# Kernel optimization log

Measured on AMD Instinct MI355X. Metric: run time of the kernel, lower is better.

Reference implementation:

```python
import jax, jax.numpy as jnp
import numpy as np

N_NODES = 50000
IN_CH = 128
OUT_CH = 64
HID = 2 * OUT_CH  # 128
N_EDGES = 800000


def _glorot(key, shape):
    fan_in, fan_out = shape[0], shape[-1]
    lim = jnp.sqrt(6.0 / (fan_in + fan_out))
    return jax.random.uniform(key, shape, jnp.float32, -lim, lim)


def setup_inputs() -> dict:
    key = jax.random.key(0)
    ks = jax.random.split(key, 10)
    x = jax.random.normal(ks[0], (N_NODES, IN_CH), jnp.float32)
    edge_index = jax.random.randint(ks[1], (2, N_EDGES), 0, N_NODES, jnp.int32)
    return {
        "x": x,
        "edge_index": edge_index,
        "W1": _glorot(ks[2], (IN_CH, HID)),
        "a_src1": _glorot(ks[3], (HID,)),
        "a_dst1": _glorot(ks[4], (HID,)),
        "b1": jnp.zeros((HID,), jnp.float32),
        "W2": _glorot(ks[5], (HID, OUT_CH)),
        "a_src2": _glorot(ks[6], (OUT_CH,)),
        "a_dst2": _glorot(ks[7], (OUT_CH,)),
        "b2": jnp.zeros((OUT_CH,), jnp.float32),
    }


def _gat_conv(x, src, dst, W, a_src, a_dst, b, n_nodes):
    # Linear transform: [N, F_out]
    h = x @ W
    # Per-node attention halves (heads=1): alpha_i = <h_i, a>
    al_s = h @ a_src  # [N]
    al_d = h @ a_dst  # [N]
    # Edge scores with LeakyReLU(0.2), PyG default negative slope
    e = jax.nn.leaky_relu(al_s[src] + al_d[dst], negative_slope=0.2)
    # Segment softmax over incoming edges of each dst node
    m = jax.ops.segment_max(e, dst, num_segments=n_nodes)
    m = jnp.where(jnp.isfinite(m), m, 0.0)
    ex = jnp.exp(e - m[dst])
    denom = jax.ops.segment_sum(ex, dst, num_segments=n_nodes)
    alpha = ex / (denom[dst] + 1e-16)  # [E]
    # Weighted scatter-add aggregation
    out = jax.ops.segment_sum(h[src] * alpha[:, None], dst, num_segments=n_nodes)
    return out + b


def reference(x, edge_index, W1, a_src1, a_dst1, b1, W2, a_src2, a_dst2, b2):
    n = x.shape[0]
    # add_self_loops=True (PyG GATConv default)
    loops = jnp.arange(n, dtype=edge_index.dtype)
    src = jnp.concatenate([edge_index[0], loops])
    dst = jnp.concatenate([edge_index[1], loops])
    h = _gat_conv(x.astype(jnp.float32), src, dst, W1, a_src1, a_dst1, b1, n)
    h = jax.nn.relu(h)
    return _gat_conv(h, src, dst, W2, a_src2, a_dst2, b2, n)
```

## Files before the change

kernel.cpp:

```cpp
#include <hip/hip_runtime.h>
#include <hip/hip_bf16.h>

#define N_NODES 50000
#define IN_CH 128
#define HID 128
#define OUT_CH 64
#define N_EDGES 800000
#define N_TOT_EDGES (N_EDGES + N_NODES)
#define ET_PAD (N_TOT_EDGES + 3 * N_NODES)
#define MPAD 50048
#define NBN ((N_NODES + 255) / 256)
#define NB_ET ((N_TOT_EDGES + 255) / 256)
#define NB_GEMM (MPAD / 64)
#define NSH 128
#define EPS (N_EDGES / NSH)
#define NDW (N_NODES / 4)

typedef float float4v __attribute__((ext_vector_type(4)));
typedef unsigned uint4v __attribute__((ext_vector_type(4)));
typedef __attribute__((ext_vector_type(8))) short bf16x8;
typedef __attribute__((ext_vector_type(4))) float f32x4;

__device__ __forceinline__ unsigned bf16_rne(float f) {
    unsigned u = __float_as_uint(f);
    return (u + 0x7fffu + ((u >> 16) & 1u)) >> 16;
}
__device__ __forceinline__ unsigned pack2(float a, float b) {
    return bf16_rne(a) | (bf16_rne(b) << 16);
}

__global__ __launch_bounds__(256) void k_pre(
        const float* __restrict__ W1, unsigned short* __restrict__ Wl1,
        const float* __restrict__ W2, unsigned short* __restrict__ Wl2) {
    const int b = blockIdx.x, t = threadIdx.x;
    const float* W; unsigned short* Wl; int N, bb;
    if (b < 8) { W = W1; Wl = Wl1; N = 128; bb = b; }
    else       { W = W2; Wl = Wl2; N = 64;  bb = b - 8; }
    const int tg = bb * 256 + t;
    if (tg >= 16 * N) return;
    const int kg = tg / N, col = tg & (N - 1);
    float v[8];
    #pragma unroll
    for (int j = 0; j < 8; ++j) v[j] = W[(size_t)(kg * 8 + j) * N + col];
    uint4 p;
    p.x = pack2(v[0], v[1]); p.y = pack2(v[2], v[3]);
    p.z = pack2(v[4], v[5]); p.w = pack2(v[6], v[7]);
    *(uint4*)&Wl[(size_t)tg * 8] = p;
}

template<int N, bool AF32, bool USELDS>
__device__ __forceinline__ void gemm_body(int gb, int t,
        const float* __restrict__ Xf, const unsigned short* __restrict__ Xb,
        const unsigned short* __restrict__ Wlg,
        const float* __restrict__ asrc, const float* __restrict__ adst,
        unsigned short* __restrict__ Hb, float* __restrict__ als,
        float* __restrict__ ald, int M, unsigned short* Wl) {
    constexpr int NF = N / 16;
    const unsigned short* Wsrc;
    if constexpr (USELDS) {
        for (int i = t; i < N * 16; i += 256)
            ((uint4*)Wl)[i] = ((const uint4*)Wlg)[i];
        __syncthreads();
        Wsrc = Wl;
    } else {
        Wsrc = Wlg;
    }

    const int lane = t & 63, w = t >> 6;
    const int rb = gb * 64 + w * 16;
    const int cl = lane & 15, g = lane >> 4;

    f32x4 acc[NF];
    #pragma unroll
    for (int n = 0; n < NF; ++n) acc[n] = (f32x4){0.f, 0.f, 0.f, 0.f};

    const float* Xrow = nullptr;
    const unsigned short* Abase = nullptr;
    if constexpr (AF32) {
        const int arow = (rb + cl < M) ? (rb + cl) : (M - 1);
        Xrow = Xf + (size_t)arow * 128;
    } else {
        Abase = Xb + (size_t)(rb >> 4) * 2048 + cl * 8;
    }

    #pragma unroll
    for (int s = 0; s < 4; ++s) {
        bf16x8 af;
        if constexpr (AF32) {
            const int k0 = (s * 4 + g) * 8;
            float4 a = *(const float4*)&Xrow[k0];
            float4 c = *(const float4*)&Xrow[k0 + 4];
            uint4v uu;
            uu[0] = pack2(a.x, a.y); uu[1] = pack2(a.z, a.w);
            uu[2] = pack2(c.x, c.y); uu[3] = pack2(c.z, c.w);
            af = __builtin_bit_cast(bf16x8, uu);
        } else {
            af = *(const bf16x8*)(Abase + (s * 4 + g) * 128);
        }
        #pragma unroll
        for (int n = 0; n < NF; ++n) {
            bf16x8 bf = *(const bf16x8*)(Wsrc + ((s * 4 + g) * N + n * 16 + cl) * 8);
            acc[n] = __builtin_amdgcn_mfma_f32_16x16x32_bf16(af, bf, acc[n], 0, 0, 0);
        }
    }

    float asv[NF], adv[NF];
    #pragma unroll
    for (int n = 0; n < NF; ++n) {
        asv[n] = asrc[n * 16 + cl];
        adv[n] = adst[n * 16 + cl];
    }

    #pragma unroll
    for (int r = 0; r < 4; ++r) {
        float ps = 0.f, pd = 0.f;
        #pragma unroll
        for (int n = 0; n < NF; ++n) {
            ps += acc[n][r] * asv[n];
            pd += acc[n][r] * adv[n];
        }
        #pragma unroll
        for (int mask = 1; mask < 16; mask <<= 1) {
            ps += __shfl_xor(ps, mask);
            pd += __shfl_xor(pd, mask);
        }
        const int row = rb + g * 4 + r;
        if (cl == 0 && row < M) { als[row] = ps; ald[row] = pd; }
    }

    #pragma unroll
    for (int r = 0; r < 4; ++r) {
        const int row = rb + g * 4 + r;
        if (row >= M) continue;
        #pragma unroll
        for (int n = 0; n < NF; ++n)
            Hb[(size_t)(n >> 1) * (size_t)M * 32 + (size_t)row * 32
               + (n & 1) * 16 + cl] = (unsigned short)bf16_rne(acc[n][r]);
    }
}

__global__ __launch_bounds__(256) void k_par1(
        const int* __restrict__ ei, unsigned* __restrict__ cnt_s,
        unsigned char* __restrict__ rank8,
        const float* __restrict__ X, const unsigned short* __restrict__ Wl1,
        const float* __restrict__ asrc, const float* __restrict__ adst,
        unsigned short* __restrict__ Hb, float* __restrict__ als,
        float* __restrict__ ald, int M) {
    __shared__ unsigned lcnt[NDW];
    const int b = blockIdx.x, t = threadIdx.x;
    if (b < NSH) {
        const int s = b;
        for (int i = t; i < NDW; i += 256) lcnt[i] = 0;
        __syncthreads();
        const int base = s * EPS;
        const int* __restrict__ dst = ei + N_EDGES;
        for (int j = base + t; j < base + EPS; j += 256) {
            int d = __builtin_nontemporal_load(&dst[j]);
            unsigned sh = 8u * (d & 3);
            unsigned old = atomicAdd(&lcnt[d >> 2], 1u << sh);
            rank8[j] = (unsigned char)((old >> sh) & 0xFFu);
        }
        __syncthreads();
        unsigned* __restrict__ outp = cnt_s + (size_t)s * NDW;
        for (int i = t; i < NDW; i += 256) outp[i] = lcnt[i];
        return;
    }
    gemm_body<HID, true, false>(b - NSH, t, X, nullptr, Wl1,
                                asrc, adst, Hb, als, ald, M, nullptr);
}

__global__ void k_scan1(const unsigned* __restrict__ cnt_s, int* __restrict__ cntT,
                        unsigned char* __restrict__ pcoff8,
                        int* __restrict__ off, int* __restrict__ bsum, int n) {
    __shared__ int s[256];
    int t = threadIdx.x;
    int i = blockIdx.x * 256 + t;
    int padded = 0;
    if (i < n) {
        const int dw = i >> 2;
        const unsigned sh = 8u * (i & 3);
        int pc = 1;
        for (int c = 0; c < NSH; ++c) {
            pcoff8[(size_t)c * n + i] = (unsigned char)pc;
            pc += (int)((cnt_s[(size_t)c * NDW + dw] >> sh) & 0xFFu);
        }
        cntT[i] = pc;
        padded = (pc + 3) & ~3;
    }
    s[t] = padded;
    __syncthreads();
    for (int d = 1; d < 256; d <<= 1) {
        int x = (t >= d) ? s[t - d] : 0;
        __syncthreads();
        s[t] += x;
        __syncthreads();
    }
    if (i < n) off[i + 1] = s[t];
    if (t == 255) bsum[blockIdx.x] = s[255];
}

__global__ void k_scan3(int* __restrict__ off, const int* __restrict__ bsum, int n) {
    __shared__ int s[256];
    int t = threadIdx.x;
    s[t] = (t < NBN) ? bsum[t] : 0;
    __syncthreads();
    for (int d = 1; d < 256; d <<= 1) {
        int x = (t >= d) ? s[t - d] : 0;
        __syncthreads();
        s[t] += x;
        __syncthreads();
    }
    int base = (blockIdx.x > 0) ? s[blockIdx.x - 1] : 0;
    int i = blockIdx.x * 256 + t;
    if (i < n) off[i + 1] += base;
    if (i == 0) off[0] = 0;
}

__global__ void k_fill2(const int* __restrict__ ei, const int* __restrict__ off,
                        const unsigned char* __restrict__ rank8,
                        const unsigned char* __restrict__ pcoff8,
                        int* __restrict__ csr, int e, int n) {
    int i = blockIdx.x * 256 + threadIdx.x;
    if (i < e) {
        int src = __builtin_nontemporal_load(&ei[i]);
        int dst = __builtin_nontemporal_load(&ei[e + i]);
        int c = i / EPS;
        int pos = off[dst] + (int)pcoff8[(size_t)c * n + dst] + (int)rank8[i];
        csr[pos] = src;
    } else if (i < e + n) {
        int v = i - e;
        csr[off[v]] = v;
    }
}

__global__ __launch_bounds__(256) void gemm_mfma64(
        const unsigned short* __restrict__ Xb, const unsigned short* __restrict__ Wlg,
        const float* __restrict__ asrc, const float* __restrict__ adst,
        unsigned short* __restrict__ Hb, float* __restrict__ als,
        float* __restrict__ ald, int M) {
    __shared__ unsigned short Wl[16 * 64 * 8];
    gemm_body<OUT_CH, false, true>(blockIdx.x, threadIdx.x, nullptr, Xb, Wlg,
                                   asrc, adst, Hb, als, ald, M, Wl);
}

template<bool PADZ>
__global__ __launch_bounds__(256) void k_edgew(
        const float* __restrict__ als, const float* __restrict__ ald,
        const int* __restrict__ off, const int* __restrict__ cntT,
        const int* __restrict__ csr,
        unsigned* __restrict__ ew, float* __restrict__ invden, int n) {
    const int fl = threadIdx.x & 15;
    const int v = blockIdx.x * 16 + (threadIdx.x >> 4);
    if (v >= n) return;
    const int start = off[v], end = start + cntT[v];
    const float aldv = ald[v];
    float s = 0.f;
    for (int j = start + fl; j < end; j += 16) {
        int src = __builtin_nontemporal_load(&csr[j]);
        float e = als[src] + aldv;
        e = e > 0.f ? e : 0.2f * e;
        unsigned r = bf16_rne(__expf(e));
        ew[j] = ((unsigned)src << 16) | r;
        s += __uint_as_float(r << 16);
    }
    if (PADZ) {
        const int pend = off[v + 1];
        for (int j = end + fl; j < pend; j += 16) ew[j] = 0;
    }
    #pragma unroll
    for (int d = 1; d < 16; d <<= 1) s += __shfl_xor(s, d);
    if (fl == 0) invden[v] = 1.f / (s + 1e-16f);
}

template<int F, bool RELU, bool PACKOUT>
__global__ __launch_bounds__(256) void k_spmm_b(
        const unsigned short* __restrict__ Hb, const unsigned* __restrict__ ew,
        const float* __restrict__ invden, const float* __restrict__ bias,
        const int* __restrict__ off, void* __restrict__ outv, int n) {
    constexpr int NCH = F / 32;
    const int chunk = blockIdx.x % NCH;
    const int v = (blockIdx.x / NCH) * 64 + (threadIdx.x >> 2);
    if (v >= n) return;
    const int q = threadIdx.x & 3;
    const int start = off[v], end = off[v + 1];
    const unsigned short* __restrict__ Hch = Hb + (size_t)chunk * (size_t)n * 32 + q * 8;

    float a0[8] = {}, a1[8] = {}, a2[8] = {}, a3[8] = {};

    #define GATB(E, A)                                                   \
        {                                                                \
            float w_ = __uint_as_float((E) << 16);                       \
            uint4 h_ = *(const uint4*)&Hch[(size_t)((E) >> 16) * 32];    \
            A[0] += w_ * __uint_as_float(h_.x << 16);                    \
            A[1] += w_ * __uint_as_float(h_.x & 0xffff0000u);            \
            A[2] += w_ * __uint_as_float(h_.y << 16);                    \
            A[3] += w_ * __uint_as_float(h_.y & 0xffff0000u);            \
            A[4] += w_ * __uint_as_float(h_.z << 16);                    \
            A[5] += w_ * __uint_as_float(h_.z & 0xffff0000u);            \
            A[6] += w_ * __uint_as_float(h_.w << 16);                    \
            A[7] += w_ * __uint_as_float(h_.w & 0xffff0000u);            \
        }
    #define GATB4(Q) GATB((Q).x, a0) GATB((Q).y, a1) GATB((Q).z, a2) GATB((Q).w, a3)

    int j = start;
    for (; j + 4 < end; j += 8) {
        uint4 eA = *(const uint4*)&ew[j];
        uint4 eB = *(const uint4*)&ew[j + 4];
        GATB4(eA)
        GATB4(eB)
    }
    if (j < end) {
        uint4 eA = *(const uint4*)&ew[j];
        GATB4(eA)
    }
    #undef GATB4
    #undef GATB

    const float inv = invden[v];
    const float* __restrict__ bp = bias + chunk * 32 + q * 8;
    float s[8];
    #pragma unroll
    for (int i = 0; i < 8; ++i) {
        s[i] = (a0[i] + a1[i] + a2[i] + a3[i]) * inv + bp[i];
        if (RELU) s[i] = fmaxf(s[i], 0.f);
    }

    if (PACKOUT) {
        unsigned short* Xb2 = (unsigned short*)outv;
        const int kg = chunk * 4 + q;
        uint4v p;
        p[0] = pack2(s[0], s[1]); p[1] = pack2(s[2], s[3]);
        p[2] = pack2(s[4], s[5]); p[3] = pack2(s[6], s[7]);
        __builtin_nontemporal_store(p,
            (uint4v*)&Xb2[(size_t)(v >> 4) * 2048 + kg * 128 + (v & 15) * 8]);
    } else {
        float* out = (float*)outv;
        float4v o0, o1;
        o0[0] = s[0]; o0[1] = s[1]; o0[2] = s[2]; o0[3] = s[3];
        o1[0] = s[4]; o1[1] = s[5]; o1[2] = s[6]; o1[3] = s[7];
        float* op = out + (size_t)v * F + chunk * 32 + q * 8;
        __builtin_nontemporal_store(o0, (float4v*)op);
        __builtin_nontemporal_store(o1, (float4v*)(op + 4));
    }
}


extern "C" void kernel_launch(void* const* d_in, const int* in_sizes, int n_in,
                              void* d_out, int out_size, void* d_ws, size_t ws_size,
                              hipStream_t stream) {
    const float* x     = (const float*)d_in[0];
    const int*   ei    = (const int*)d_in[1];
    const float* W1    = (const float*)d_in[2];
    const float* as1   = (const float*)d_in[3];
    const float* ad1   = (const float*)d_in[4];
    const float* b1    = (const float*)d_in[5];
    const float* W2    = (const float*)d_in[6];
    const float* as2   = (const float*)d_in[7];
    const float* ad2   = (const float*)d_in[8];
    const float* b2    = (const float*)d_in[9];
    float* out = (float*)d_out;

    const int Nn = N_NODES;

    char* ws = (char*)d_ws;
    size_t o = 0;
    auto carve = [&](size_t bytes) { char* p = ws + o; o = (o + bytes + 255) & ~(size_t)255; return p; };
    int*            off   = (int*)carve((Nn + 1) * sizeof(int));
    int*            cntT  = (int*)carve(Nn * sizeof(int));
    int*            bsum  = (int*)carve(256 * sizeof(int));
    unsigned char*  rank8 = (unsigned char*)carve((size_t)N_EDGES);
    unsigned*       cnt_s = (unsigned*)carve((size_t)NSH * NDW * sizeof(unsigned));
    unsigned char*  pcoff8= (unsigned char*)carve((size_t)NSH * Nn);
    int*            csr   = (int*)carve((size_t)ET_PAD * sizeof(int));
    unsigned*       ew    = (unsigned*)carve((size_t)ET_PAD * sizeof(unsigned));
    unsigned short* h1b   = (unsigned short*)carve((size_t)Nn * HID * sizeof(unsigned short));
    unsigned short* h2b   = (unsigned short*)carve((size_t)Nn * OUT_CH * sizeof(unsigned short));
    unsigned short* Xb2   = (unsigned short*)carve((size_t)MPAD * 128 * sizeof(unsigned short));
    unsigned short* Wl1   = (unsigned short*)carve(16 * 128 * 8 * sizeof(unsigned short));
    unsigned short* Wl2   = (unsigned short*)carve(16 * 64 * 8 * sizeof(unsigned short));
    float*          als   = (float*)carve(Nn * sizeof(float));
    float*          ald   = (float*)carve(Nn * sizeof(float));
    float*          invd  = (float*)carve(Nn * sizeof(float));

    k_pre<<<12, 256, 0, stream>>>(W1, Wl1, W2, Wl2);

    k_par1<<<NSH + NB_GEMM, 256, 0, stream>>>(
        ei, cnt_s, rank8, x, Wl1, as1, ad1, h1b, als, ald, Nn);

    k_scan1<<<NBN, 256, 0, stream>>>(cnt_s, cntT, pcoff8, off, bsum, Nn);
    k_scan3<<<NBN, 256, 0, stream>>>(off, bsum, Nn);

    k_fill2<<<NB_ET, 256, 0, stream>>>(ei, off, rank8, pcoff8, csr, N_EDGES, Nn);

    const int nbEW  = (Nn + 15) / 16;
    const int nbN64 = (Nn + 63) / 64;

    k_edgew<true><<<nbEW, 256, 0, stream>>>(als, ald, off, cntT, csr, ew, invd, Nn);
    k_spmm_b<HID, true, true><<<nbN64 * (HID / 32), 256, 0, stream>>>(
        h1b, ew, invd, b1, off, Xb2, Nn);

    gemm_mfma64<<<NB_GEMM, 256, 0, stream>>>(
        Xb2, Wl2, as2, ad2, h2b, als, ald, Nn);
    k_edgew<false><<<nbEW, 256, 0, stream>>>(als, ald, off, cntT, csr, ew, invd, Nn);
    k_spmm_b<OUT_CH, false, false><<<nbN64 * (OUT_CH / 32), 256, 0, stream>>>(
        h2b, ew, invd, b2, off, out, Nn);
}
```

Measured before the change: 152.3 us.

## Fuse layer-1 edge weight computation into CSR fill and drop csr array

The CSR fill kernel now computes the layer-1 attention exp weight directly and writes the packed (src, weight) word into the edge-weight array. A separate int CSR array is no longer written. A lightweight kernel then sums the weights per node for the inverse denominator and zeroes the padding. Layer 2 reads the source index from the upper bits of the packed word and rewrites only the weight half. This removes one full pass that wrote and read back the csr array. In exchange, the fill kernel does random gathers of als/ald and adds a reduction kernel that re-reads ew.

```diff
diff --git a/kernel.cpp b/kernel.cpp
--- a/kernel.cpp
+++ b/kernel.cpp
@@ -216,21 +216,43 @@
     if (i == 0) off[0] = 0;
 }
 
-__global__ void k_fill2(const int* __restrict__ ei, const int* __restrict__ off,
+__global__ void k_fillw(const int* __restrict__ ei, const int* __restrict__ off,
                         const unsigned char* __restrict__ rank8,
                         const unsigned char* __restrict__ pcoff8,
-                        int* __restrict__ csr, int e, int n) {
+                        const float* __restrict__ als, const float* __restrict__ ald,
+                        unsigned* __restrict__ ew, int e, int n) {
     int i = blockIdx.x * 256 + threadIdx.x;
     if (i < e) {
         int src = __builtin_nontemporal_load(&ei[i]);
         int dst = __builtin_nontemporal_load(&ei[e + i]);
         int c = i / EPS;
         int pos = off[dst] + (int)pcoff8[(size_t)c * n + dst] + (int)rank8[i];
-        csr[pos] = src;
+        float ev = als[src] + ald[dst];
+        ev = ev > 0.f ? ev : 0.2f * ev;
+        ew[pos] = ((unsigned)src << 16) | bf16_rne(__expf(ev));
     } else if (i < e + n) {
         int v = i - e;
-        csr[off[v]] = v;
-    }
+        float ev = als[v] + ald[v];
+        ev = ev > 0.f ? ev : 0.2f * ev;
+        ew[off[v]] = ((unsigned)v << 16) | bf16_rne(__expf(ev));
+    }
+}
+
+__global__ __launch_bounds__(256) void k_inv(
+        const int* __restrict__ off, const int* __restrict__ cntT,
+        unsigned* __restrict__ ew, float* __restrict__ invden, int n) {
+    const int fl = threadIdx.x & 15;
+    const int v = blockIdx.x * 16 + (threadIdx.x >> 4);
+    if (v >= n) return;
+    const int start = off[v], end = start + cntT[v];
+    const int pend = off[v + 1];
+    float s = 0.f;
+    for (int j = start + fl; j < end; j += 16)
+        s += __uint_as_float(ew[j] << 16);
+    for (int j = end + fl; j < pend; j += 16) ew[j] = 0;
+    #pragma unroll
+    for (int d = 1; d < 16; d <<= 1) s += __shfl_xor(s, d);
+    if (fl == 0) invden[v] = 1.f / (s + 1e-16f);
 }
 
 __global__ __launch_bounds__(256) void gemm_mfma64(
@@ -243,11 +265,9 @@
                                    asrc, adst, Hb, als, ald, M, Wl);
 }
 
-template<bool PADZ>
-__global__ __launch_bounds__(256) void k_edgew(
+__global__ __launch_bounds__(256) void k_edgew2(
         const float* __restrict__ als, const float* __restrict__ ald,
         const int* __restrict__ off, const int* __restrict__ cntT,
-        const int* __restrict__ csr,
         unsigned* __restrict__ ew, float* __restrict__ invden, int n) {
     const int fl = threadIdx.x & 15;
     const int v = blockIdx.x * 16 + (threadIdx.x >> 4);
@@ -256,16 +276,13 @@
     const float aldv = ald[v];
     float s = 0.f;
     for (int j = start + fl; j < end; j += 16) {
-        int src = __builtin_nontemporal_load(&csr[j]);
+        unsigned old = ew[j];
+        int src = (int)(old >> 16);
         float e = als[src] + aldv;
         e = e > 0.f ? e : 0.2f * e;
         unsigned r = bf16_rne(__expf(e));
-        ew[j] = ((unsigned)src << 16) | r;
+        ew[j] = (old & 0xFFFF0000u) | r;
         s += __uint_as_float(r << 16);
-    }
-    if (PADZ) {
-        const int pend = off[v + 1];
-        for (int j = end + fl; j < pend; j += 16) ew[j] = 0;
     }
     #pragma unroll
     for (int d = 1; d < 16; d <<= 1) s += __shfl_xor(s, d);
@@ -371,7 +388,6 @@
     unsigned char*  rank8 = (unsigned char*)carve((size_t)N_EDGES);
     unsigned*       cnt_s = (unsigned*)carve((size_t)NSH * NDW * sizeof(unsigned));
     unsigned char*  pcoff8= (unsigned char*)carve((size_t)NSH * Nn);
-    int*            csr   = (int*)carve((size_t)ET_PAD * sizeof(int));
     unsigned*       ew    = (unsigned*)carve((size_t)ET_PAD * sizeof(unsigned));
     unsigned short* h1b   = (unsigned short*)carve((size_t)Nn * HID * sizeof(unsigned short));
     unsigned short* h2b   = (unsigned short*)carve((size_t)Nn * OUT_CH * sizeof(unsigned short));
@@ -390,18 +406,20 @@
     k_scan1<<<NBN, 256, 0, stream>>>(cnt_s, cntT, pcoff8, off, bsum, Nn);
     k_scan3<<<NBN, 256, 0, stream>>>(off, bsum, Nn);
 
-    k_fill2<<<NB_ET, 256, 0, stream>>>(ei, off, rank8, pcoff8, csr, N_EDGES, Nn);
+    k_fillw<<<NB_ET, 256, 0, stream>>>(ei, off, rank8, pcoff8, als, ald,
+                                       ew, N_EDGES, Nn);
 
     const int nbEW  = (Nn + 15) / 16;
     const int nbN64 = (Nn + 63) / 64;
 
-    k_edgew<true><<<nbEW, 256, 0, stream>>>(als, ald, off, cntT, csr, ew, invd, Nn);
+    k_inv<<<nbEW, 256, 0, stream>>>(off, cntT, ew, invd, Nn);
+
     k_spmm_b<HID, true, true><<<nbN64 * (HID / 32), 256, 0, stream>>>(
         h1b, ew, invd, b1, off, Xb2, Nn);
 
     gemm_mfma64<<<NB_GEMM, 256, 0, stream>>>(
         Xb2, Wl2, as2, ad2, h2b, als, ald, Nn);
-    k_edgew<false><<<nbEW, 256, 0, stream>>>(als, ald, off, cntT, csr, ew, invd, Nn);
+    k_edgew2<<<nbEW, 256, 0, stream>>>(als, ald, off, cntT, ew, invd, Nn);
     k_spmm_b<OUT_CH, false, false><<<nbN64 * (OUT_CH / 32), 256, 0, stream>>>(
         h2b, ew, invd, b2, off, out, Nn);
 }
```

Result: faster. 147.9 us (-2.9%).
